# Kernel tuning notes

Measured on AMD Instinct MI355X. Metric: run time of the kernel, lower is better.

## Reference

```python
import jax, jax.numpy as jnp
import numpy as np

HEADS = 8
DIM_HEAD = 40
SCALE = DIM_HEAD ** -0.5


def setup_inputs() -> dict:
    key = jax.random.key(0)
    ks = jax.random.split(key, 6)
    B, S, D = 2, 4096, 320  # batch, seq (64x64 latent), query_dim
    inner = HEADS * DIM_HEAD  # 320
    s = 0.02
    return {
        "x": jax.random.normal(ks[0], (B, S, D), jnp.float32),
        "Wq": jax.random.normal(ks[1], (inner, D), jnp.float32) * s,
        "Wk": jax.random.normal(ks[2], (inner, D), jnp.float32) * s,
        "Wv": jax.random.normal(ks[3], (inner, D), jnp.float32) * s,
        "Wout": jax.random.normal(ks[4], (D, inner), jnp.float32) * s,
        "bout": jnp.zeros((D,), jnp.float32),
    }


def _split_heads(t):
    # [B, S, h*d] -> [B, h, S, d]
    B, S, _ = t.shape
    return t.reshape(B, S, HEADS, DIM_HEAD).transpose(0, 2, 1, 3)


def reference(x, Wq, Wk, Wv, Wout, bout):
    # self-attention path (context=None): k/v come from x
    q = _split_heads(x @ Wq.T)  # [B,h,S,d]
    k = _split_heads(x @ Wk.T)
    v = _split_heads(x @ Wv.T)
    # scores: materialized O(S^2) attention as in the torch einsum
    attn = jax.nn.softmax(jnp.einsum('bhid,bhjd->bhij', q, k) * SCALE, axis=-1)
    out = jnp.einsum('bhij,bhjd->bhid', attn, v)  # [B,h,S,d]
    B, _, S, _ = out.shape
    out = out.transpose(0, 2, 1, 3).reshape(B, S, HEADS * DIM_HEAD)
    return out @ Wout.T + bout  # to_out (dropout=0 -> identity)
```

## Files before the change

### kernel.cpp

```cpp
#include <hip/hip_runtime.h>

#define HEADS 8
#define DHEAD 40
#define SEQ   4096
#define BATCH 2
#define INNER 320
#define NBH   16
#define QSCALE ((float)(0.15811388300841897 * 1.4426950408889634))

typedef _Float16 f16;
typedef __attribute__((ext_vector_type(2)))  __fp16   fp16x2;
typedef __attribute__((ext_vector_type(4)))  _Float16 half4;
typedef __attribute__((ext_vector_type(8)))  _Float16 half8;
typedef __attribute__((ext_vector_type(16))) float    f32x16;

#if __has_builtin(__builtin_amdgcn_exp2f)
#define EXP2F(x) __builtin_amdgcn_exp2f(x)
#else
#define EXP2F(x) exp2f(x)
#endif

union H8 { half8 h8; fp16x2 p2[4]; uint4 u4; };

#define XN4   (BATCH * SEQ * INNER / 4)
#define WQKV4 (3 * INNER * INNER / 4)
#define WOUT4 (INNER * INNER / 4)
#define CONV_TOTAL (XN4 + WQKV4 + WOUT4)

__global__ __launch_bounds__(256)
void convert_kernel(const float* __restrict__ x,
                    const float* __restrict__ Wq,
                    const float* __restrict__ Wk,
                    const float* __restrict__ Wv,
                    const float* __restrict__ Wout,
                    f16* __restrict__ xh, f16* __restrict__ wh,
                    f16* __restrict__ wouth)
{
    int i = blockIdx.x * 256 + threadIdx.x;
    if (i >= CONV_TOTAL) return;
    float4 v;
    f16* dst;
    float sc = 1.0f;
    if (i < XN4) {
        v = ((const float4*)x)[i];
        dst = xh + 4 * (size_t)i;
    } else if (i < XN4 + WQKV4) {
        int j = i - XN4;
        if (j < 25600)      { v = ((const float4*)Wq)[j]; sc = QSCALE; }
        else if (j < 51200) { v = ((const float4*)Wk)[j - 25600]; }
        else                { v = ((const float4*)Wv)[j - 51200]; }
        dst = wh + 4 * (size_t)j;
    } else {
        int j = i - XN4 - WQKV4;
        v = ((const float4*)Wout)[j];
        dst = wouth + 4 * (size_t)j;
    }
    H8 u;
    u.p2[0] = __builtin_amdgcn_cvt_pkrtz(v.x * sc, v.y * sc);
    u.p2[1] = __builtin_amdgcn_cvt_pkrtz(v.z * sc, v.w * sc);
    *(uint2*)dst = make_uint2(u.u4.x, u.u4.y);
}

#define QSTR 72

__global__ __launch_bounds__(256)
void qkv_gemm_kernel(const f16* __restrict__ xh, const f16* __restrict__ wh,
                     f16* __restrict__ q, f16* __restrict__ k,
                     f16* __restrict__ vt)
{
    __shared__ f16 lds[(64 + 192) * QSTR];
    f16* As = lds;
    f16* Bs = lds + 64 * QSTR;

    const int tid = threadIdx.x;
    const int nb0 = blockIdx.x * 64;
    const int m0  = blockIdx.y * 64;
    const int wave = tid >> 6, lane = tid & 63, m = lane & 31, half = lane >> 5;
    const int mw = wave >> 1, nw = wave & 1;

    f32x16 acc[3];
    #pragma unroll
    for (int i = 0; i < 16; i++) { acc[0][i] = 0.f; acc[1][i] = 0.f; acc[2][i] = 0.f; }

    for (int k0 = 0; k0 < 320; k0 += 64) {
        __syncthreads();
        #pragma unroll
        for (int u = 0; u < 2; u++) {
            int idx = tid + 256 * u;
            int r = idx >> 3, c8 = idx & 7;
            *(uint4*)&As[r * QSTR + c8 * 8] =
                *(const uint4*)&xh[(size_t)(m0 + r) * 320 + k0 + c8 * 8];
        }
        #pragma unroll
        for (int u = 0; u < 6; u++) {
            int idx = tid + 256 * u;
            int r = idx >> 3, c8 = idx & 7;
            int wr = (r >> 6) * 320 + nb0 + (r & 63);
            *(uint4*)&Bs[r * QSTR + c8 * 8] =
                *(const uint4*)&wh[(size_t)wr * 320 + k0 + c8 * 8];
        }
        __syncthreads();
        #pragma unroll
        for (int c = 0; c < 4; c++) {
            half8 a = *(const half8*)&As[(mw * 32 + m) * QSTR + c * 16 + half * 8];
            #pragma unroll
            for (int t = 0; t < 3; t++) {
                half8 bf = *(const half8*)&Bs[(nw * 96 + t * 32 + m) * QSTR + c * 16 + half * 8];
                acc[t] = __builtin_amdgcn_mfma_f32_32x32x16_f16(a, bf, acc[t], 0, 0, 0);
            }
        }
    }

    const int b = m0 >> 12, s0 = m0 & 4095;

    #pragma unroll
    for (int t = 0; t < 3; t++) {
        int st = nw * 3 + t;
        if (st < 4) {
            f16* dst = (st < 2) ? q : k;
            int col = nb0 + (st & 1) * 32 + m;
            int h  = (col * 205) >> 13;
            int dd = col - h * 40;
            #pragma unroll
            for (int reg = 0; reg < 16; reg++) {
                int crow = 4 * half + (reg & 3) + 8 * (reg >> 2);
                int mg = m0 + mw * 32 + crow;
                int bb = mg >> 12, s = mg & 4095;
                dst[((size_t)(bb * 8 + h) * SEQ + s) * DHEAD + dd] = (f16)acc[t][reg];
            }
        }
    }

    __syncthreads();
    f16* Ct = lds;
    if (nw == 1) {
        #pragma unroll
        for (int t = 1; t < 3; t++) {
            int vr0 = (t - 1) * 32 + m;
            #pragma unroll
            for (int g = 0; g < 4; g++) {
                half4 hh;
                hh.x = (f16)acc[t][4 * g + 0]; hh.y = (f16)acc[t][4 * g + 1];
                hh.z = (f16)acc[t][4 * g + 2]; hh.w = (f16)acc[t][4 * g + 3];
                *(half4*)&Ct[vr0 * QSTR + mw * 32 + 8 * g + 4 * half] = hh;
            }
        }
    }
    __syncthreads();
    #pragma unroll
    for (int u = 0; u < 4; u++) {
        int idx = tid + 256 * u;
        int rl = idx >> 4, c4 = idx & 15;
        int col = nb0 + rl;
        int h  = (col * 205) >> 13;
        int dd = col - h * 40;
        int w4 = c4 & 3;
        int c4p = (c4 & ~3) | ((w4 == 1) ? 2 : (w4 == 2) ? 1 : w4);
        *(uint2*)&vt[((size_t)(b * 8 + h) * DHEAD + dd) * SEQ + s0 + c4p * 4] =
            *(const uint2*)&Ct[rl * QSTR + c4 * 4];
    }
}

#define KSTR 56
#define VSTR 72
#define LDS_K 0
#define LDS_V 3584

__global__ __launch_bounds__(256, 4)
void attn_kernel(const f16* __restrict__ q, const f16* __restrict__ k,
                 const f16* __restrict__ vt, f16* __restrict__ y)
{
    __shared__ __align__(16) unsigned char ldsbuf[16896];
    f16*   ldsh = (f16*)ldsbuf;
    float* ldsf = (float*)ldsbuf;

    const int tid = threadIdx.x;
    const int blk = blockIdx.x;
    const int bh = blk >> 6, qt = blk & 63;
    const int b = bh >> 3, h = bh & 7;
    const int q0 = qt * 64;
    const int wave = tid >> 6, lane = tid & 63, m = lane & 31, half = lane >> 5;
    const int qs = wave >> 1, kh = wave & 1;

    if (tid < 128) {
        int key = tid >> 1, off = (tid & 1) * 4;
        *(uint2*)&ldsh[LDS_K + key * KSTR + 40 + off] = make_uint2(0u, 0u);
    }
    for (int i = tid; i < 24 * 16; i += 256) {
        int r = i >> 4, c = (i & 15) * 4;
        uint2 val = (r == 0) ? make_uint2(0x3C003C00u, 0x3C003C00u)
                             : make_uint2(0u, 0u);
        *(uint2*)&ldsh[LDS_V + (40 + r) * VSTR + c] = val;
    }

    half8 zero8;
    #pragma unroll
    for (int j = 0; j < 8; j++) zero8[j] = (f16)0.0f;
    half8 qa[3];
    {
        const f16* qb = q + ((size_t)bh * SEQ + q0 + qs * 32 + m) * DHEAD;
        qa[0] = *(const half8*)&qb[half * 8];
        qa[1] = *(const half8*)&qb[16 + half * 8];
        qa[2] = (half == 1) ? zero8 : *(const half8*)&qb[32];
    }

    f32x16 O[2];
    #pragma unroll
    for (int i = 0; i < 16; i++) { O[0][i] = 0.f; O[1][i] = 0.f; }

    const f16* kb = k  + (size_t)bh * SEQ * DHEAD;
    const f16* vb = vt + (size_t)bh * DHEAD * SEQ;

    const int krow0 = tid / 5,          kblk0 = tid % 5;
    const int krow1 = (256 + tid) / 5,  kblk1 = (256 + tid) % 5;
    const int vrow0 = tid >> 3,         vblk0 = tid & 7;
    const int vrow1 = (256 + tid) >> 3, vblk1 = (256 + tid) & 7;
    const bool lo64 = (tid < 64);

    uint4 ka0, ka1, va0, va1;
    ka0 = *(const uint4*)&kb[(size_t)krow0 * DHEAD + kblk0 * 8];
    va0 = *(const uint4*)&vb[(size_t)vrow0 * SEQ + vblk0 * 8];
    if (lo64) {
        ka1 = *(const uint4*)&kb[(size_t)krow1 * DHEAD + kblk1 * 8];
        va1 = *(const uint4*)&vb[(size_t)vrow1 * SEQ + vblk1 * 8];
    }

    for (int j0 = 0; j0 < SEQ; j0 += 64) {
        __syncthreads();
        *(uint4*)&ldsh[LDS_K + krow0 * KSTR + kblk0 * 8] = ka0;
        *(uint4*)&ldsh[LDS_V + vrow0 * VSTR + vblk0 * 8] = va0;
        if (lo64) {
            *(uint4*)&ldsh[LDS_K + krow1 * KSTR + kblk1 * 8] = ka1;
            *(uint4*)&ldsh[LDS_V + vrow1 * VSTR + vblk1 * 8] = va1;
        }
        __syncthreads();

        if (j0 + 64 < SEQ) {
            const int jn = j0 + 64;
            ka0 = *(const uint4*)&kb[(size_t)(jn + krow0) * DHEAD + kblk0 * 8];
            va0 = *(const uint4*)&vb[(size_t)vrow0 * SEQ + jn + vblk0 * 8];
            if (lo64) {
                ka1 = *(const uint4*)&kb[(size_t)(jn + krow1) * DHEAD + kblk1 * 8];
                va1 = *(const uint4*)&vb[(size_t)vrow1 * SEQ + jn + vblk1 * 8];
            }
        }

        f32x16 S;
        #pragma unroll
        for (int i = 0; i < 16; i++) S[i] = 0.f;
        #pragma unroll
        for (int c = 0; c < 3; c++) {
            half8 kf = *(const half8*)&ldsh[LDS_K + (kh * 32 + m) * KSTR + c * 16 + half * 8];
            S = __builtin_amdgcn_mfma_f32_32x32x16_f16(kf, qa[c], S, 0, 0, 0);
        }

        H8 p0u, p1u;
        #pragma unroll
        for (int g = 0; g < 4; g++) {
            p0u.p2[g] = __builtin_amdgcn_cvt_pkrtz(EXP2F(S[2 * g]),     EXP2F(S[2 * g + 1]));
            p1u.p2[g] = __builtin_amdgcn_cvt_pkrtz(EXP2F(S[8 + 2 * g]), EXP2F(S[9 + 2 * g]));
        }

        #pragma unroll
        for (int c = 0; c < 2; c++) {
            half8 pc = c ? p1u.h8 : p0u.h8;
            half8 v0 = *(const half8*)&ldsh[LDS_V + m * VSTR + kh * 32 + c * 16 + half * 8];
            half8 v1 = *(const half8*)&ldsh[LDS_V + (32 + m) * VSTR + kh * 32 + c * 16 + half * 8];
            O[0] = __builtin_amdgcn_mfma_f32_32x32x16_f16(pc, v0, O[0], 0, 0, 0);
            O[1] = __builtin_amdgcn_mfma_f32_32x32x16_f16(pc, v1, O[1], 0, 0, 0);
        }
    }

    __syncthreads();
    if (kh == 1) {
        #pragma unroll
        for (int t = 0; t < 2; t++)
            #pragma unroll
            for (int reg = 0; reg < 16; reg++) {
                int row = 4 * half + (reg & 3) + 8 * (reg >> 2);
                ldsf[(qs * 32 + row) * 66 + t * 32 + m] = O[t][reg];
            }
    }
    __syncthreads();
    if (kh == 0) {
        #pragma unroll
        for (int t = 0; t < 2; t++)
            #pragma unroll
            for (int reg = 0; reg < 16; reg++) {
                int row = 4 * half + (reg & 3) + 8 * (reg >> 2);
                O[t][reg] += ldsf[(qs * 32 + row) * 66 + t * 32 + m];
            }
        #pragma unroll
        for (int reg = 0; reg < 16; reg++) {
            float l = __shfl(O[1][reg], 8 + 32 * half, 64);
            float rinv = 1.0f / l;
            int row = 4 * half + (reg & 3) + 8 * (reg >> 2);
            f16* yr = y + ((size_t)b * SEQ + q0 + qs * 32 + row) * INNER + h * DHEAD;
            yr[m] = (f16)(O[0][reg] * rinv);
            if (m < 8) yr[32 + m] = (f16)(O[1][reg] * rinv);
        }
    }
}

#define ASTR 72

__global__ __launch_bounds__(256)
void out_proj_kernel(const f16* __restrict__ y, const f16* __restrict__ wouth,
                     const float* __restrict__ bout, float* __restrict__ out)
{
    __shared__ f16 lds[(128 + 64) * ASTR];
    f16* As = lds;
    f16* Bs = lds + 128 * ASTR;

    const int tid = threadIdx.x;
    const int m0 = blockIdx.y * 128;
    const int n0 = blockIdx.x * 64;
    const int wave = tid >> 6, lane = tid & 63, m = lane & 31, half = lane >> 5;

    f32x16 acc[2];
    #pragma unroll
    for (int i = 0; i < 16; i++) { acc[0][i] = 0.f; acc[1][i] = 0.f; }

    for (int k0 = 0; k0 < 320; k0 += 64) {
        __syncthreads();
        #pragma unroll
        for (int u = 0; u < 4; u++) {
            int idx = tid + 256 * u;
            int r = idx >> 3, c8 = idx & 7;
            *(uint4*)&As[r * ASTR + c8 * 8] =
                *(const uint4*)&y[(size_t)(m0 + r) * 320 + k0 + c8 * 8];
        }
        #pragma unroll
        for (int u = 0; u < 2; u++) {
            int idx = tid + 256 * u;
            int r = idx >> 3, c8 = idx & 7;
            *(uint4*)&Bs[r * ASTR + c8 * 8] =
                *(const uint4*)&wouth[(size_t)(n0 + r) * 320 + k0 + c8 * 8];
        }
        __syncthreads();
        #pragma unroll
        for (int c = 0; c < 4; c++) {
            half8 a  = *(const half8*)&As[(wave * 32 + m) * ASTR + c * 16 + half * 8];
            half8 b0 = *(const half8*)&Bs[m * ASTR + c * 16 + half * 8];
            half8 b1 = *(const half8*)&Bs[(32 + m) * ASTR + c * 16 + half * 8];
            acc[0] = __builtin_amdgcn_mfma_f32_32x32x16_f16(a, b0, acc[0], 0, 0, 0);
            acc[1] = __builtin_amdgcn_mfma_f32_32x32x16_f16(a, b1, acc[1], 0, 0, 0);
        }
    }

    #pragma unroll
    for (int nt = 0; nt < 2; nt++) {
        int n = n0 + nt * 32 + m;
        float bias = bout[n];
        #pragma unroll
        for (int reg = 0; reg < 16; reg++) {
            int crow = 4 * half + (reg & 3) + 8 * (reg >> 2);
            out[(size_t)(m0 + wave * 32 + crow) * 320 + n] = acc[nt][reg] + bias;
        }
    }
}

extern "C" void kernel_launch(void* const* d_in, const int* in_sizes, int n_in,
                              void* d_out, int out_size, void* d_ws, size_t ws_size,
                              hipStream_t stream)
{
    const float* x    = (const float*)d_in[0];
    const float* Wq   = (const float*)d_in[1];
    const float* Wk   = (const float*)d_in[2];
    const float* Wv   = (const float*)d_in[3];
    const float* Wout = (const float*)d_in[4];
    const float* bout = (const float*)d_in[5];
    float* out = (float*)d_out;

    unsigned char* ws = (unsigned char*)d_ws;
    f16* xh    = (f16*)(ws);
    f16* wh    = (f16*)(ws +  5242880);
    f16* wouth = (f16*)(ws +  5857280);
    f16* qd    = (f16*)(ws +  6062080);
    f16* kd    = (f16*)(ws + 11304960);
    f16* vtd   = (f16*)(ws + 16547840);
    f16* yd    = (f16*)(ws + 21790720);

    convert_kernel <<<2960,         256, 0, stream>>>(x, Wq, Wk, Wv, Wout, xh, wh, wouth);
    qkv_gemm_kernel<<<dim3(5, 128), 256, 0, stream>>>(xh, wh, qd, kd, vtd);
    attn_kernel    <<<1024,         256, 0, stream>>>(qd, kd, vtd, yd);
    out_proj_kernel<<<dim3(5, 64),  256, 0, stream>>>(yd, wouth, bout, out);
}
```

Before: 165.9 us.

## Load K/V fragments directly from global into registers, drop LDS staging

The attention kernel no longer stages K and V tiles through shared memory with two barriers per iteration. Each wave instead loads its MFMA operand fragments straight from global memory, prefetching K one tile ahead, and synthesizes the ones row for the softmax denominator in registers. Block indices are also remapped so that blocks of the same batch-head land on the same XCD for L2 locality, and s_setprio is wrapped around the MFMA groups. This removes LDS traffic and synchronization, but each wave now issues redundant global/L2 reads and V loads are not prefetched ahead of use.

```diff
diff --git a/kernel.cpp b/kernel.cpp
--- a/kernel.cpp
+++ b/kernel.cpp
@@ -161,41 +161,25 @@
     }
 }
 
-#define KSTR 56
-#define VSTR 72
-#define LDS_K 0
-#define LDS_V 3584
-
 __global__ __launch_bounds__(256, 4)
 void attn_kernel(const f16* __restrict__ q, const f16* __restrict__ k,
                  const f16* __restrict__ vt, f16* __restrict__ y)
 {
-    __shared__ __align__(16) unsigned char ldsbuf[16896];
-    f16*   ldsh = (f16*)ldsbuf;
-    float* ldsf = (float*)ldsbuf;
+    __shared__ float ldsf[64 * 66];
 
     const int tid = threadIdx.x;
     const int blk = blockIdx.x;
-    const int bh = blk >> 6, qt = blk & 63;
+    const int xcd = blk & 7, slot = blk >> 3;
+    const int bh = xcd * 2 + (slot >> 6), qt = slot & 63;
     const int b = bh >> 3, h = bh & 7;
     const int q0 = qt * 64;
     const int wave = tid >> 6, lane = tid & 63, m = lane & 31, half = lane >> 5;
     const int qs = wave >> 1, kh = wave & 1;
 
-    if (tid < 128) {
-        int key = tid >> 1, off = (tid & 1) * 4;
-        *(uint2*)&ldsh[LDS_K + key * KSTR + 40 + off] = make_uint2(0u, 0u);
-    }
-    for (int i = tid; i < 24 * 16; i += 256) {
-        int r = i >> 4, c = (i & 15) * 4;
-        uint2 val = (r == 0) ? make_uint2(0x3C003C00u, 0x3C003C00u)
-                             : make_uint2(0u, 0u);
-        *(uint2*)&ldsh[LDS_V + (40 + r) * VSTR + c] = val;
-    }
-
-    half8 zero8;
-    #pragma unroll
-    for (int j = 0; j < 8; j++) zero8[j] = (f16)0.0f;
+    half8 zero8, ones8;
+    #pragma unroll
+    for (int j = 0; j < 8; j++) { zero8[j] = (f16)0.0f; ones8[j] = (f16)1.0f; }
+
     half8 qa[3];
     {
         const f16* qb = q + ((size_t)bh * SEQ + q0 + qs * 32 + m) * DHEAD;
@@ -211,47 +195,39 @@
     const f16* kb = k  + (size_t)bh * SEQ * DHEAD;
     const f16* vb = vt + (size_t)bh * DHEAD * SEQ;
 
-    const int krow0 = tid / 5,          kblk0 = tid % 5;
-    const int krow1 = (256 + tid) / 5,  kblk1 = (256 + tid) % 5;
-    const int vrow0 = tid >> 3,         vblk0 = tid & 7;
-    const int vrow1 = (256 + tid) >> 3, vblk1 = (256 + tid) & 7;
-    const bool lo64 = (tid < 64);
-
-    uint4 ka0, ka1, va0, va1;
-    ka0 = *(const uint4*)&kb[(size_t)krow0 * DHEAD + kblk0 * 8];
-    va0 = *(const uint4*)&vb[(size_t)vrow0 * SEQ + vblk0 * 8];
-    if (lo64) {
-        ka1 = *(const uint4*)&kb[(size_t)krow1 * DHEAD + kblk1 * 8];
-        va1 = *(const uint4*)&vb[(size_t)vrow1 * SEQ + vblk1 * 8];
-    }
+    const f16* kl  = kb + (size_t)(kh * 32 + m) * DHEAD + half * 8;
+    const f16* v0l = vb + (size_t)m * SEQ + kh * 32 + half * 8;
+    const f16* v1l = vb + (size_t)(32 + (m & 7)) * SEQ + kh * 32 + half * 8;
+
+    half8 kf0 = *(const half8*)(kl);
+    half8 kf1 = *(const half8*)(kl + 16);
+    half8 kf2 = *(const half8*)(kl + 32);
 
     for (int j0 = 0; j0 < SEQ; j0 += 64) {
-        __syncthreads();
-        *(uint4*)&ldsh[LDS_K + krow0 * KSTR + kblk0 * 8] = ka0;
-        *(uint4*)&ldsh[LDS_V + vrow0 * VSTR + vblk0 * 8] = va0;
-        if (lo64) {
-            *(uint4*)&ldsh[LDS_K + krow1 * KSTR + kblk1 * 8] = ka1;
-            *(uint4*)&ldsh[LDS_V + vrow1 * VSTR + vblk1 * 8] = va1;
-        }
-        __syncthreads();
+        const f16* v0p = v0l + j0;
+        const f16* v1p = v1l + j0;
+        half8 va00 = *(const half8*)(v0p);
+        half8 va01 = *(const half8*)(v0p + 16);
+        half8 va10 = zero8, va11 = zero8;
+        if (m < 8) {
+            va10 = *(const half8*)(v1p);
+            va11 = *(const half8*)(v1p + 16);
+        }
+
+        f32x16 S;
+        #pragma unroll
+        for (int i = 0; i < 16; i++) S[i] = 0.f;
+        __builtin_amdgcn_s_setprio(1);
+        S = __builtin_amdgcn_mfma_f32_32x32x16_f16(kf0, qa[0], S, 0, 0, 0);
+        S = __builtin_amdgcn_mfma_f32_32x32x16_f16(kf1, qa[1], S, 0, 0, 0);
+        S = __builtin_amdgcn_mfma_f32_32x32x16_f16(kf2, qa[2], S, 0, 0, 0);
+        __builtin_amdgcn_s_setprio(0);
 
         if (j0 + 64 < SEQ) {
-            const int jn = j0 + 64;
-            ka0 = *(const uint4*)&kb[(size_t)(jn + krow0) * DHEAD + kblk0 * 8];
-            va0 = *(const uint4*)&vb[(size_t)vrow0 * SEQ + jn + vblk0 * 8];
-            if (lo64) {
-                ka1 = *(const uint4*)&kb[(size_t)(jn + krow1) * DHEAD + kblk1 * 8];
-                va1 = *(const uint4*)&vb[(size_t)vrow1 * SEQ + jn + vblk1 * 8];
-            }
-        }
-
-        f32x16 S;
-        #pragma unroll
-        for (int i = 0; i < 16; i++) S[i] = 0.f;
-        #pragma unroll
-        for (int c = 0; c < 3; c++) {
-            half8 kf = *(const half8*)&ldsh[LDS_K + (kh * 32 + m) * KSTR + c * 16 + half * 8];
-            S = __builtin_amdgcn_mfma_f32_32x32x16_f16(kf, qa[c], S, 0, 0, 0);
+            const f16* kp = kl + (size_t)(j0 + 64) * DHEAD;
+            kf0 = *(const half8*)(kp);
+            kf1 = *(const half8*)(kp + 16);
+            kf2 = *(const half8*)(kp + 32);
         }
 
         H8 p0u, p1u;
@@ -261,17 +237,16 @@
             p1u.p2[g] = __builtin_amdgcn_cvt_pkrtz(EXP2F(S[8 + 2 * g]), EXP2F(S[9 + 2 * g]));
         }
 
-        #pragma unroll
-        for (int c = 0; c < 2; c++) {
-            half8 pc = c ? p1u.h8 : p0u.h8;
-            half8 v0 = *(const half8*)&ldsh[LDS_V + m * VSTR + kh * 32 + c * 16 + half * 8];
-            half8 v1 = *(const half8*)&ldsh[LDS_V + (32 + m) * VSTR + kh * 32 + c * 16 + half * 8];
-            O[0] = __builtin_amdgcn_mfma_f32_32x32x16_f16(pc, v0, O[0], 0, 0, 0);
-            O[1] = __builtin_amdgcn_mfma_f32_32x32x16_f16(pc, v1, O[1], 0, 0, 0);
-        }
-    }
-
-    __syncthreads();
+        half8 w0 = (m == 8) ? ones8 : va10;
+        half8 w1 = (m == 8) ? ones8 : va11;
+        __builtin_amdgcn_s_setprio(1);
+        O[0] = __builtin_amdgcn_mfma_f32_32x32x16_f16(p0u.h8, va00, O[0], 0, 0, 0);
+        O[1] = __builtin_amdgcn_mfma_f32_32x32x16_f16(p0u.h8, w0,   O[1], 0, 0, 0);
+        O[0] = __builtin_amdgcn_mfma_f32_32x32x16_f16(p1u.h8, va01, O[0], 0, 0, 0);
+        O[1] = __builtin_amdgcn_mfma_f32_32x32x16_f16(p1u.h8, w1,   O[1], 0, 0, 0);
+        __builtin_amdgcn_s_setprio(0);
+    }
+
     if (kh == 1) {
         #pragma unroll
         for (int t = 0; t < 2; t++)
```

Result: slower. 210.2 us (+26.7%).
